# Performance work log

Hardware: AMD Instinct MI355X
Metric: run time of the kernel (lower is better)

The kernel has to match this reference:

```python
import jax, jax.numpy as jnp
import numpy as np

N_NODES = 100000
IN_CH = 256
EMBED = 256
N_EDGES = 300000
EPS = 1e-5


def _glorot(key, shape):
    fan_in, fan_out = shape[0], shape[1]
    lim = (6.0 / (fan_in + fan_out)) ** 0.5
    return jax.random.uniform(key, shape, jnp.float32, -lim, lim)


def setup_inputs() -> dict:
    key = jax.random.key(0)
    ks = jax.random.split(key, 16)
    inp = {}
    inp['node_feat'] = jax.random.normal(ks[0], (N_NODES, IN_CH), jnp.float32)
    inp['src'] = jax.random.randint(ks[1], (N_EDGES,), 0, N_NODES, jnp.int32)
    inp['dst'] = jax.random.randint(ks[2], (N_EDGES,), 0, N_NODES, jnp.int32)
    inp['neg'] = jax.random.randint(ks[3], (N_EDGES,), 0, N_NODES, jnp.int32)
    # GCNConv weights (x @ W + b), 3 layers
    inp['W1'] = _glorot(ks[4], (IN_CH, EMBED)); inp['b1'] = jnp.zeros((EMBED,), jnp.float32)
    inp['W2'] = _glorot(ks[5], (EMBED, EMBED)); inp['b2'] = jnp.zeros((EMBED,), jnp.float32)
    inp['W3'] = _glorot(ks[6], (EMBED, EMBED)); inp['b3'] = jnp.zeros((EMBED,), jnp.float32)
    # BatchNorm affine params (2 BN layers)
    inp['g1'] = jnp.ones((EMBED,), jnp.float32); inp['be1'] = jnp.zeros((EMBED,), jnp.float32)
    inp['g2'] = jnp.ones((EMBED,), jnp.float32); inp['be2'] = jnp.zeros((EMBED,), jnp.float32)
    # LinkPredictor MLP
    inp['fc1_w'] = _glorot(ks[7], (2 * EMBED, EMBED)); inp['fc1_b'] = jnp.zeros((EMBED,), jnp.float32)
    inp['fc2_w'] = _glorot(ks[8], (EMBED, 1)); inp['fc2_b'] = jnp.zeros((1,), jnp.float32)
    return inp


def gcn_conv(x, W, b, src, dst, n):
    # PyG GCNConv: out = D^{-1/2} (A + I) D^{-1/2} (x @ W) + b
    xw = x @ W
    loops = jnp.arange(n, dtype=src.dtype)
    src_l = jnp.concatenate([src, loops])
    dst_l = jnp.concatenate([dst, loops])
    deg = jax.ops.segment_sum(jnp.ones_like(dst_l, jnp.float32), dst_l, num_segments=n)
    dinv = jnp.where(deg > 0, jax.lax.rsqrt(deg), 0.0)
    norm = dinv[src_l] * dinv[dst_l]  # [E+N]
    msg = norm[:, None] * xw[src_l]   # [E+N, d]
    out = jax.ops.segment_sum(msg, dst_l, num_segments=n)
    return out + b


def batch_norm(x, g, b):
    # training-mode BN over node dim, biased variance (torch semantics)
    mu = jnp.mean(x, axis=0)
    var = jnp.mean((x - mu) ** 2, axis=0)
    return (x - mu) * jax.lax.rsqrt(var + EPS) * g + b


def link_pred(z_a, z_b, fc1_w, fc1_b, fc2_w, fc2_b):
    h = jnp.concatenate([z_a, z_b], axis=1) @ fc1_w + fc1_b
    h = jax.nn.relu(h)
    return jax.nn.sigmoid(h @ fc2_w + fc2_b).reshape(-1)


def reference(node_feat, src, dst, neg, W1, b1, W2, b2, W3, b3, g1, be1, g2, be2, fc1_w, fc1_b, fc2_w, fc2_b):
    n = node_feat.shape[0]
    # encoder (dropout p used only in training; inference/deterministic here)
    x = gcn_conv(node_feat, W1, b1, src, dst, n)
    x = jax.nn.relu(batch_norm(x, g1, be1))
    x = gcn_conv(x, W2, b2, src, dst, n)
    x = jax.nn.relu(batch_norm(x, g2, be2))
    z = gcn_conv(x, W3, b3, src, dst, n)
    z_src, z_dst, z_neg = z[src], z[dst], z[neg]
    pos_out = link_pred(z_src, z_dst, fc1_w, fc1_b, fc2_w, fc2_b)
    neg_out = link_pred(z_src, z_neg, fc1_w, fc1_b, fc2_w, fc2_b)
    return (pos_out, neg_out)
```

## Files before the change

kernel.cpp:

```cpp
#include <hip/hip_runtime.h>
#include <hip/hip_bf16.h>

#define N_NODES 100000
#define N_EDGES 300000
#define CH 256
#define EPS 1e-5f
#define AGG_BLOCKS 3125
#define Y_TILES 782
#define Y_TILES_PAD 784
#define CAST_CHUNK 5000

typedef __hip_bfloat16 bf16;
typedef __attribute__((ext_vector_type(8))) short bf16x8_t;
typedef __attribute__((ext_vector_type(4))) float f32x4_t;

__device__ __forceinline__ unsigned short f2bf(float f) {
    bf16 h = __float2bfloat16(f);
    return __builtin_bit_cast(unsigned short, h);
}
__device__ __forceinline__ float bflo(unsigned int w) {
    return __builtin_bit_cast(float, w << 16);
}
__device__ __forceinline__ float bfhi(unsigned int w) {
    return __builtin_bit_cast(float, w & 0xffff0000u);
}
__device__ __forceinline__ unsigned pack2(float a, float b) {
    return (unsigned)f2bf(a) | ((unsigned)f2bf(b) << 16);
}
__device__ __forceinline__ void store_val(bf16* p, float v) { *p = __float2bfloat16(v); }

__device__ __forceinline__ void async_copy16(const void* g, void* l) {
    __builtin_amdgcn_global_load_lds((const __attribute__((address_space(1))) void*)g,
                                     (__attribute__((address_space(3))) void*)l, 16, 0, 0);
}

__device__ __forceinline__ void cast_chunk(const float* __restrict__ x,
                                           unsigned short* __restrict__ y, int i) {
    float4 v = ((const float4*)x)[i];
    ushort4 o;
    o.x = f2bf(v.x); o.y = f2bf(v.y); o.z = f2bf(v.z); o.w = f2bf(v.w);
    ((ushort4*)y)[i] = o;
}

__global__ void k_zero_int(int* __restrict__ p, int n,
                           const float* __restrict__ cx, unsigned short* __restrict__ cy,
                           int castBase, int nbMain) {
    if ((int)blockIdx.x >= nbMain) {
        cast_chunk(cx, cy, (castBase + (int)blockIdx.x - nbMain) * 256 + (int)threadIdx.x);
        return;
    }
    int i = blockIdx.x * 256 + threadIdx.x;
    if (i < n) p[i] = 0;
}
__global__ void k_count_deg(const int* __restrict__ dst, int* __restrict__ deg,
                            const float* __restrict__ cx, unsigned short* __restrict__ cy,
                            int castBase, int nbMain) {
    if ((int)blockIdx.x >= nbMain) {
        cast_chunk(cx, cy, (castBase + (int)blockIdx.x - nbMain) * 256 + (int)threadIdx.x);
        return;
    }
    int e = blockIdx.x * 256 + threadIdx.x;
    if (e < N_EDGES) atomicAdd(&deg[dst[e]], 1);
}
__global__ void k_block_sums(const int* __restrict__ deg, int* __restrict__ bsum,
                             float* __restrict__ dinv,
                             const float* __restrict__ cx, unsigned short* __restrict__ cy,
                             int castBase, int nbMain) {
    if ((int)blockIdx.x >= nbMain) {
        cast_chunk(cx, cy, (castBase + (int)blockIdx.x - nbMain) * 256 + (int)threadIdx.x);
        return;
    }
    __shared__ int s[256];
    int t = threadIdx.x;
    int i = blockIdx.x * 256 + t;
    int v = (i < N_NODES) ? deg[i] : 0;
    s[t] = v;
    if (i < N_NODES) dinv[i] = rsqrtf((float)(v + 1));
    __syncthreads();
    for (int off = 128; off > 0; off >>= 1) {
        if (t < off) s[t] += s[t + off];
        __syncthreads();
    }
    if (t == 0) bsum[blockIdx.x] = s[0];
}
__global__ void k_scan_bsums(int* __restrict__ bsum, int nb) {
    __shared__ int s[512];
    int t = threadIdx.x;
    int v = (t < nb) ? bsum[t] : 0;
    s[t] = v;
    __syncthreads();
    for (int off = 1; off < 512; off <<= 1) {
        int u = (t >= off) ? s[t - off] : 0;
        __syncthreads();
        s[t] += u;
        __syncthreads();
    }
    if (t < nb) bsum[t] = s[t] - v;
}
__global__ void k_row_ptr(const int* __restrict__ deg, const int* __restrict__ bsum,
                          int* __restrict__ row_ptr,
                          const float* __restrict__ cx, unsigned short* __restrict__ cy,
                          int castBase, int nbMain) {
    if ((int)blockIdx.x >= nbMain) {
        cast_chunk(cx, cy, (castBase + (int)blockIdx.x - nbMain) * 256 + (int)threadIdx.x);
        return;
    }
    __shared__ int s[256];
    int t = threadIdx.x;
    int i = blockIdx.x * 256 + t;
    int v = (i < N_NODES) ? deg[i] : 0;
    s[t] = v;
    __syncthreads();
    for (int off = 1; off < 256; off <<= 1) {
        int u = (t >= off) ? s[t - off] : 0;
        __syncthreads();
        s[t] += u;
        __syncthreads();
    }
    if (i < N_NODES) row_ptr[i] = bsum[blockIdx.x] + s[t] - v;
    if (blockIdx.x == 0 && t == 0) row_ptr[N_NODES] = N_EDGES;
}
__global__ void k_scatter(const int* __restrict__ src, const int* __restrict__ dst,
                          const int* __restrict__ row_ptr, int* __restrict__ cursor,
                          const float* __restrict__ dinv,
                          int* __restrict__ col, float* __restrict__ wedge,
                          int* __restrict__ eid, int* __restrict__ rowid,
                          const float* __restrict__ cx, unsigned short* __restrict__ cy,
                          int castBase, int nbMain) {
    if ((int)blockIdx.x >= nbMain) {
        cast_chunk(cx, cy, (castBase + (int)blockIdx.x - nbMain) * 256 + (int)threadIdx.x);
        return;
    }
    int e = blockIdx.x * 256 + threadIdx.x;
    if (e < N_EDGES) {
        int d = dst[e], s = src[e];
        int p = atomicAdd(&cursor[d], 1);
        int idx = row_ptr[d] + p;
        col[idx] = s;
        wedge[idx] = dinv[d] * dinv[s];
        eid[idx] = e;
        rowid[idx] = d;
    }
}

__global__ void k_transpose_all(const float* __restrict__ W1, const float* __restrict__ W2,
                                bf16* __restrict__ wt) {
    int which = blockIdx.x >> 8;
    int idx = ((blockIdx.x & 255) << 8) + threadIdx.x;
    int n = idx >> 8, k = idx & 255;
    const float* W = which ? W2 : W1;
    wt[(size_t)which * 65536 + (size_t)n * 256 + k] =
        __float2bfloat16(W[(size_t)k * 256 + n]);
}

__global__ void k_fuse_w(const float* __restrict__ W3, const float* __restrict__ fc1w,
                         const float* __restrict__ b3, const float* __restrict__ fc1b,
                         bf16* __restrict__ wtf, float* __restrict__ bout) {
    int n = threadIdx.x;
    int nc = n & 255;
    size_t ro = (n < 256) ? 0 : 256;
    if (blockIdx.x == 256) {
        float acc = (n < 256) ? fc1b[n] : 0.f;
#pragma unroll 4
        for (int j = 0; j < 256; ++j)
            acc += b3[j] * fc1w[(ro + j) * 256 + nc];
        bout[n] = acc;
        return;
    }
    __shared__ float w3row[256];
    int k = blockIdx.x;
    if (n < 256) w3row[n] = W3[(size_t)k * 256 + n];
    __syncthreads();
    float acc = 0.f;
#pragma unroll 4
    for (int j = 0; j < 256; ++j)
        acc += w3row[j] * fc1w[(ro + j) * 256 + nc];
    wtf[(size_t)n * 256 + k] = __float2bfloat16(acc);
}

template <int NX, bool BIAS, bool STATS>
__global__ __launch_bounds__(256) void k_gemm_mfma(const bf16* __restrict__ A,
                                                   const bf16* __restrict__ Bt,
                                                   bf16* __restrict__ C, int M, int ldc,
                                                   const float* __restrict__ bias,
                                                   float* __restrict__ part) {
    constexpr int LOG2NX = (NX == 4) ? 2 : 1;
    int id = blockIdx.x;
    int rg = (id & 7) + 8 * (id >> (3 + LOG2NX));
    int ct = (id >> 3) & (NX - 1);
    if (rg >= Y_TILES) return;
    const int row0 = rg * 128;
    const int col0 = ct * 128;

    __shared__ bf16 As[2 * 128 * 64];
    __shared__ bf16 Bs[2 * 128 * 64];
    __shared__ float sS[2][128];
    __shared__ float sQ[2][128];
    const int tid = threadIdx.x;
    const int lane = tid & 63;
    const int w = tid >> 6;
    const int wr = w >> 1, wc = w & 1;
    const int lr = lane & 15, quad = lane >> 4;

    f32x4_t acc[4][4] = {};

    auto issue_ab = [&](int k0, int buf) {
#pragma unroll
        for (int i = 0; i < 4; ++i) {
            int j = i * 256 + tid;
            int r = j >> 3, c = j & 7;
            int gk = ((c ^ (r & 7)) << 3);
            int gr = row0 + r; gr = gr < M ? gr : M - 1;
            async_copy16(A + (size_t)gr * 256 + k0 + gk, (void*)(As + buf * 8192 + j * 8));
            async_copy16(Bt + (size_t)(col0 + r) * 256 + k0 + gk,
                         (void*)(Bs + buf * 8192 + j * 8));
        }
    };
    auto compute = [&](int buf) {
#pragma unroll
        for (int ks = 0; ks < 2; ++ks) {
            bf16x8_t af[4], bfr[4];
#pragma unroll
            for (int mi = 0; mi < 4; ++mi) {
                int m = wr * 64 + mi * 16 + lr;
                int c = (ks * 4 + quad) ^ (m & 7);
                af[mi] = *(const bf16x8_t*)(As + buf * 8192 + m * 64 + c * 8);
            }
#pragma unroll
            for (int ni = 0; ni < 4; ++ni) {
                int n = wc * 64 + ni * 16 + lr;
                int c = (ks * 4 + quad) ^ (n & 7);
                bfr[ni] = *(const bf16x8_t*)(Bs + buf * 8192 + n * 64 + c * 8);
            }
#pragma unroll
            for (int mi = 0; mi < 4; ++mi)
#pragma unroll
                for (int ni = 0; ni < 4; ++ni)
                    acc[mi][ni] = __builtin_amdgcn_mfma_f32_16x16x32_bf16(
                        af[mi], bfr[ni], acc[mi][ni], 0, 0, 0);
        }
    };

    issue_ab(0, 0);

#pragma unroll
    for (int k = 0; k < 4; ++k) {
        const int cur = k & 1;
        if (k < 3) issue_ab((k + 1) * 64, cur ^ 1);
        __builtin_amdgcn_sched_barrier(0);
        if (k < 3) asm volatile("s_waitcnt vmcnt(8)" ::: "memory");
        else asm volatile("s_waitcnt vmcnt(0)" ::: "memory");
        __builtin_amdgcn_sched_barrier(0);
        __builtin_amdgcn_s_barrier();
        compute(cur);
        __builtin_amdgcn_s_barrier();
        __builtin_amdgcn_sched_barrier(0);
    }

#pragma unroll
    for (int ni = 0; ni < 4; ++ni) {
        int colg = col0 + wc * 64 + ni * 16 + lr;
        float bv = BIAS ? bias[colg] : 0.f;
#pragma unroll
        for (int mi = 0; mi < 4; ++mi)
#pragma unroll
            for (int r = 0; r < 4; ++r) acc[mi][ni][r] += bv;
    }
    if (STATS) {
        float cs[4] = {}, cq[4] = {};
#pragma unroll
        for (int mi = 0; mi < 4; ++mi)
#pragma unroll
            for (int r = 0; r < 4; ++r) {
                int row = row0 + wr * 64 + mi * 16 + quad * 4 + r;
                if (row < M) {
#pragma unroll
                    for (int ni = 0; ni < 4; ++ni) {
                        float v = acc[mi][ni][r];
                        cs[ni] += v;
                        cq[ni] += v * v;
                    }
                }
            }
#pragma unroll
        for (int ni = 0; ni < 4; ++ni) {
            cs[ni] += __shfl_xor(cs[ni], 16, 64);
            cs[ni] += __shfl_xor(cs[ni], 32, 64);
            cq[ni] += __shfl_xor(cq[ni], 16, 64);
            cq[ni] += __shfl_xor(cq[ni], 32, 64);
        }
        if (quad == 0) {
#pragma unroll
            for (int ni = 0; ni < 4; ++ni) {
                int cc = wc * 64 + ni * 16 + lr;
                sS[wr][cc] = cs[ni];
                sQ[wr][cc] = cq[ni];
            }
        }
        __syncthreads();
        if (tid < 128) {
            float ss = sS[0][tid] + sS[1][tid];
            float qq = sQ[0][tid] + sQ[1][tid];
            int cg = col0 + tid;
            part[(size_t)rg * 512 + cg] = ss;
            part[(size_t)rg * 512 + 256 + cg] = qq;
        }
    }
#pragma unroll
    for (int mi = 0; mi < 4; ++mi) {
#pragma unroll
        for (int r = 0; r < 4; ++r) {
            int row = row0 + wr * 64 + mi * 16 + quad * 4 + r;
            if (row < M) {
#pragma unroll
                for (int ni = 0; ni < 4; ++ni) {
                    int colg = col0 + wc * 64 + ni * 16 + lr;
                    store_val(C + (size_t)row * ldc + colg, acc[mi][ni][r]);
                }
            }
        }
    }
}

template <bool BN>
__device__ __forceinline__ void expand8(uint4 m, const float* sc, const float* sh, float* r) {
    r[0] = bflo(m.x); r[1] = bfhi(m.x); r[2] = bflo(m.y); r[3] = bfhi(m.y);
    r[4] = bflo(m.z); r[5] = bfhi(m.z); r[6] = bflo(m.w); r[7] = bfhi(m.w);
    if (BN) {
#pragma unroll
        for (int i = 0; i < 8; ++i) r[i] = fmaxf(r[i] * sc[i] + sh[i], 0.f);
    }
}

template <bool BN, bool STATS>
__global__ __launch_bounds__(256) void k_agg_csr(const unsigned short* __restrict__ x,
                                                 const int* __restrict__ row_ptr,
                                                 const int* __restrict__ col,
                                                 const float* __restrict__ wedge,
                                                 const float* __restrict__ dinv,
                                                 const float* __restrict__ scale,
                                                 const float* __restrict__ shift,
                                                 const float* __restrict__ bias,
                                                 bf16* __restrict__ out,
                                                 float* __restrict__ part) {
    __shared__ float sred[8][256];
    __shared__ float qred[8][256];
    int g = threadIdx.x >> 5, lh = threadIdx.x & 31;
    int base = blockIdx.x * 32 + g * 4;
    const uint4* xv = (const uint4*)x;
    float sc[8], sh[8], bs[8];
    if (BN) {
        float4 a = ((const float4*)scale)[lh * 2];
        float4 b = ((const float4*)scale)[lh * 2 + 1];
        float4 c = ((const float4*)shift)[lh * 2];
        float4 d = ((const float4*)shift)[lh * 2 + 1];
        sc[0] = a.x; sc[1] = a.y; sc[2] = a.z; sc[3] = a.w;
        sc[4] = b.x; sc[5] = b.y; sc[6] = b.z; sc[7] = b.w;
        sh[0] = c.x; sh[1] = c.y; sh[2] = c.z; sh[3] = c.w;
        sh[4] = d.x; sh[5] = d.y; sh[6] = d.z; sh[7] = d.w;
    }
    if (STATS) {
        float4 e = ((const float4*)bias)[lh * 2];
        float4 f = ((const float4*)bias)[lh * 2 + 1];
        bs[0] = e.x; bs[1] = e.y; bs[2] = e.z; bs[3] = e.w;
        bs[4] = f.x; bs[5] = f.y; bs[6] = f.z; bs[7] = f.w;
    }
    float s8[8] = {}, q8[8] = {};
#pragma unroll
    for (int n = 0; n < 4; ++n) {
        int node = base + n;
        int beg = row_ptr[node], end = row_ptr[node + 1];
        float dv = dinv[node];
        float s2 = dv * dv;
        uint4 xr = xv[(size_t)node * 32 + lh];
        float rs[8];
        expand8<BN>(xr, sc, sh, rs);
        float a[8];
#pragma unroll
        for (int t = 0; t < 8; ++t) a[t] = s2 * rs[t];
        int i = beg;
        for (; i + 2 <= end; i += 2) {
            int sa = col[i], sb = col[i + 1];
            float wa = wedge[i], wb = wedge[i + 1];
            uint4 ma = xv[(size_t)sa * 32 + lh];
            uint4 mb = xv[(size_t)sb * 32 + lh];
            float ra[8], rb[8];
            expand8<BN>(ma, sc, sh, ra);
            expand8<BN>(mb, sc, sh, rb);
#pragma unroll
            for (int t = 0; t < 8; ++t) a[t] += wa * ra[t] + wb * rb[t];
        }
        if (i < end) {
            int sa = col[i];
            float wa = wedge[i];
            uint4 ma = xv[(size_t)sa * 32 + lh];
            float ra[8];
            expand8<BN>(ma, sc, sh, ra);
#pragma unroll
            for (int t = 0; t < 8; ++t) a[t] += wa * ra[t];
        }
        if (STATS) {
#pragma unroll
            for (int t = 0; t < 8; ++t) {
                a[t] += bs[t];
                s8[t] += a[t];
                q8[t] += a[t] * a[t];
            }
        }
        uint4 o;
        o.x = pack2(a[0], a[1]); o.y = pack2(a[2], a[3]);
        o.z = pack2(a[4], a[5]); o.w = pack2(a[6], a[7]);
        ((uint4*)(out + (size_t)node * CH))[lh] = o;
    }
    if (STATS) {
#pragma unroll
        for (int j = 0; j < 8; ++j) {
            sred[g][lh * 8 + j] = s8[j];
            qred[g][lh * 8 + j] = q8[j];
        }
        __syncthreads();
        int t = threadIdx.x;
        float ss = 0.f, qq = 0.f;
#pragma unroll
        for (int gg = 0; gg < 8; ++gg) {
            ss += sred[gg][t];
            qq += qred[gg][t];
        }
        part[(size_t)blockIdx.x * 512 + t] = ss;
        part[(size_t)blockIdx.x * 512 + 256 + t] = qq;
    }
}

__global__ __launch_bounds__(256) void k_bn_finalize(const float* __restrict__ part,
                                                     const float* __restrict__ g,
                                                     const float* __restrict__ be,
                                                     float* __restrict__ scale,
                                                     float* __restrict__ shift, int npart) {
    int wave = threadIdx.x >> 6, lane = threadIdx.x & 63;
    int c = blockIdx.x * 4 + wave;
    float s = 0.f, q = 0.f;
    for (int j = lane; j < npart; j += 64) {
        s += part[(size_t)j * 512 + c];
        q += part[(size_t)j * 512 + 256 + c];
    }
#pragma unroll
    for (int off = 32; off > 0; off >>= 1) {
        s += __shfl_down(s, off, 64);
        q += __shfl_down(q, off, 64);
    }
    if (lane == 0) {
        float mu = s * (1.0f / N_NODES);
        float var = q * (1.0f / N_NODES) - mu * mu;
        float sc = g[c] * rsqrtf(var + EPS);
        scale[c] = sc;
        shift[c] = be[c] - mu * sc;
    }
}

__global__ __launch_bounds__(256) void k_edge_score(
        const unsigned short* __restrict__ uv,
        const int* __restrict__ col, const int* __restrict__ eid,
        const int* __restrict__ rowid, const int* __restrict__ neg,
        const float* __restrict__ fc2_w, const float* __restrict__ fc2_b,
        float* __restrict__ out) {
    constexpr int NWG = 18750;
    constexpr int Q = NWG / 8, R = NWG % 8;
    int bid = blockIdx.x;
    int xcd = bid & 7, ord = bid >> 3;
    int swz = ((xcd < R) ? xcd * (Q + 1) : R * (Q + 1) + (xcd - R) * Q) + ord;
    int wave = threadIdx.x >> 6, lane = threadIdx.x & 63;
    int qtr = lane >> 4, l = lane & 15;
    int i = swz * 16 + wave * 4 + qtr;
    int s = col[i], d = rowid[i], e = eid[i];
    int g = neg[e];
    const uint4* uvv = (const uint4*)uv;
    uint4 u0 = uvv[(size_t)s * 64 + l * 2];
    uint4 u1 = uvv[(size_t)s * 64 + l * 2 + 1];
    uint4 p0 = uvv[(size_t)d * 64 + 32 + l * 2];
    uint4 p1 = uvv[(size_t)d * 64 + 33 + l * 2];
    uint4 n0 = uvv[(size_t)g * 64 + 32 + l * 2];
    uint4 n1 = uvv[(size_t)g * 64 + 33 + l * 2];
    float4 w0 = ((const float4*)fc2_w)[l * 4];
    float4 w1 = ((const float4*)fc2_w)[l * 4 + 1];
    float4 w2 = ((const float4*)fc2_w)[l * 4 + 2];
    float4 w3 = ((const float4*)fc2_w)[l * 4 + 3];

    float t0 = bflo(u0.x), t1 = bfhi(u0.x), t2 = bflo(u0.y), t3 = bfhi(u0.y);
    float t4 = bflo(u0.z), t5 = bfhi(u0.z), t6 = bflo(u0.w), t7 = bfhi(u0.w);
    float t8 = bflo(u1.x), t9 = bfhi(u1.x), ta = bflo(u1.y), tb = bfhi(u1.y);
    float tc = bflo(u1.z), td = bfhi(u1.z), te = bflo(u1.w), tf = bfhi(u1.w);

    float accp =
        fmaxf(t0 + bflo(p0.x), 0.f) * w0.x + fmaxf(t1 + bfhi(p0.x), 0.f) * w0.y +
        fmaxf(t2 + bflo(p0.y), 0.f) * w0.z + fmaxf(t3 + bfhi(p0.y), 0.f) * w0.w +
        fmaxf(t4 + bflo(p0.z), 0.f) * w1.x + fmaxf(t5 + bfhi(p0.z), 0.f) * w1.y +
        fmaxf(t6 + bflo(p0.w), 0.f) * w1.z + fmaxf(t7 + bfhi(p0.w), 0.f) * w1.w +
        fmaxf(t8 + bflo(p1.x), 0.f) * w2.x + fmaxf(t9 + bfhi(p1.x), 0.f) * w2.y +
        fmaxf(ta + bflo(p1.y), 0.f) * w2.z + fmaxf(tb + bfhi(p1.y), 0.f) * w2.w +
        fmaxf(tc + bflo(p1.z), 0.f) * w3.x + fmaxf(td + bfhi(p1.z), 0.f) * w3.y +
        fmaxf(te + bflo(p1.w), 0.f) * w3.z + fmaxf(tf + bfhi(p1.w), 0.f) * w3.w;
    float accn =
        fmaxf(t0 + bflo(n0.x), 0.f) * w0.x + fmaxf(t1 + bfhi(n0.x), 0.f) * w0.y +
        fmaxf(t2 + bflo(n0.y), 0.f) * w0.z + fmaxf(t3 + bfhi(n0.y), 0.f) * w0.w +
        fmaxf(t4 + bflo(n0.z), 0.f) * w1.x + fmaxf(t5 + bfhi(n0.z), 0.f) * w1.y +
        fmaxf(t6 + bflo(n0.w), 0.f) * w1.z + fmaxf(t7 + bfhi(n0.w), 0.f) * w1.w +
        fmaxf(t8 + bflo(n1.x), 0.f) * w2.x + fmaxf(t9 + bfhi(n1.x), 0.f) * w2.y +
        fmaxf(ta + bflo(n1.y), 0.f) * w2.z + fmaxf(tb + bfhi(n1.y), 0.f) * w2.w +
        fmaxf(tc + bflo(n1.z), 0.f) * w3.x + fmaxf(td + bfhi(n1.z), 0.f) * w3.y +
        fmaxf(te + bflo(n1.w), 0.f) * w3.z + fmaxf(tf + bfhi(n1.w), 0.f) * w3.w;
#pragma unroll
    for (int off = 8; off > 0; off >>= 1) {
        accp += __shfl_down(accp, off, 64);
        accn += __shfl_down(accn, off, 64);
    }
    if (l == 0) {
        float bb = fc2_b[0];
        out[e] = 1.0f / (1.0f + expf(-(accp + bb)));
        out[N_EDGES + e] = 1.0f / (1.0f + expf(-(accn + bb)));
    }
}

extern "C" void kernel_launch(void* const* d_in, const int* in_sizes, int n_in,
                              void* d_out, int out_size, void* d_ws, size_t ws_size,
                              hipStream_t stream) {
    const float* node_feat = (const float*)d_in[0];
    const int* src = (const int*)d_in[1];
    const int* dst = (const int*)d_in[2];
    const int* neg = (const int*)d_in[3];
    const float* W1 = (const float*)d_in[4];  const float* b1 = (const float*)d_in[5];
    const float* W2 = (const float*)d_in[6];  const float* b2 = (const float*)d_in[7];
    const float* W3 = (const float*)d_in[8];  const float* b3 = (const float*)d_in[9];
    const float* g1 = (const float*)d_in[10]; const float* be1 = (const float*)d_in[11];
    const float* g2 = (const float*)d_in[12]; const float* be2 = (const float*)d_in[13];
    const float* fc1_w = (const float*)d_in[14]; const float* fc1_b = (const float*)d_in[15];
    const float* fc2_w = (const float*)d_in[16]; const float* fc2_b = (const float*)d_in[17];
    float* out = (float*)d_out;

    const size_t NF = (size_t)N_NODES * CH;
    bf16* UV = (bf16*)d_ws;
    bf16* Xbf = UV + 2 * NF;
    bf16* XwBf = Xbf + NF;
    bf16* wt = XwBf + NF;
    float* dinv = (float*)(wt + 4 * 65536);
    float* bnpart = dinv + N_NODES;
    float* scale = bnpart + (size_t)AGG_BLOCKS * 512;
    float* shift = scale + CH;
    float* b3fc = shift + CH;
    float* wedge = b3fc + 512;
    int* ideg = (int*)(wedge + N_EDGES);
    int* cursor = ideg + N_NODES;
    int* row_ptr = cursor + N_NODES;
    int* col = row_ptr + N_NODES + 1;
    int* eid = col + N_EDGES;
    int* rowid = eid + N_EDGES;
    int* bsum = rowid + N_EDGES;
    (void)ws_size;

    int gemmBlocks = 2 * Y_TILES_PAD;
    int uvBlocks = 4 * Y_TILES_PAD;
    int nodeBlocks = (N_NODES + 255) / 256;
    int edgeBlocks = (N_EDGES + 255) / 256;
    int zeroBlocks = (2 * N_NODES + 255) / 256;
    int scoreBlocks = N_EDGES / 16;
    unsigned short* Xc = (unsigned short*)Xbf;

    k_zero_int<<<zeroBlocks + CAST_CHUNK, 256, 0, stream>>>(
        ideg, 2 * N_NODES, node_feat, Xc, 0 * CAST_CHUNK, zeroBlocks);
    k_count_deg<<<edgeBlocks + CAST_CHUNK, 256, 0, stream>>>(
        dst, ideg, node_feat, Xc, 1 * CAST_CHUNK, edgeBlocks);
    k_block_sums<<<nodeBlocks + CAST_CHUNK, 256, 0, stream>>>(
        ideg, bsum, dinv, node_feat, Xc, 2 * CAST_CHUNK, nodeBlocks);
    k_scan_bsums<<<1, 512, 0, stream>>>(bsum, nodeBlocks);
    k_row_ptr<<<nodeBlocks + CAST_CHUNK, 256, 0, stream>>>(
        ideg, bsum, row_ptr, node_feat, Xc, 3 * CAST_CHUNK, nodeBlocks);
    k_scatter<<<edgeBlocks + CAST_CHUNK, 256, 0, stream>>>(
        src, dst, row_ptr, cursor, dinv, col, wedge, eid, rowid,
        node_feat, Xc, 4 * CAST_CHUNK, edgeBlocks);

    k_transpose_all<<<512, 256, 0, stream>>>(W1, W2, wt);
    k_fuse_w<<<257, 512, 0, stream>>>(W3, fc1_w, b3, fc1_b, wt + 2 * 65536, b3fc);

    k_gemm_mfma<2, false, false><<<gemmBlocks, 256, 0, stream>>>(
        Xbf, wt, XwBf, N_NODES, 256, nullptr, nullptr);
    k_agg_csr<false, true><<<AGG_BLOCKS, 256, 0, stream>>>(
        (unsigned short*)XwBf, row_ptr, col, wedge, dinv, nullptr, nullptr, b1, Xbf, bnpart);
    k_bn_finalize<<<64, 256, 0, stream>>>(bnpart, g1, be1, scale, shift, AGG_BLOCKS);

    k_agg_csr<true, false><<<AGG_BLOCKS, 256, 0, stream>>>(
        (unsigned short*)Xbf, row_ptr, col, wedge, dinv, scale, shift, nullptr, XwBf, nullptr);
    k_gemm_mfma<2, true, true><<<gemmBlocks, 256, 0, stream>>>(
        XwBf, wt + 65536, Xbf, N_NODES, 256, b2, bnpart);
    k_bn_finalize<<<64, 256, 0, stream>>>(bnpart, g2, be2, scale, shift, Y_TILES);

    k_agg_csr<true, false><<<AGG_BLOCKS, 256, 0, stream>>>(
        (unsigned short*)Xbf, row_ptr, col, wedge, dinv, scale, shift, nullptr, XwBf, nullptr);
    k_gemm_mfma<4, true, false><<<uvBlocks, 256, 0, stream>>>(
        XwBf, wt + 2 * 65536, UV, N_NODES, 512, b3fc, nullptr);

    k_edge_score<<<scoreBlocks, 256, 0, stream>>>((unsigned short*)UV, col, eid, rowid, neg,
                                                  fc2_w, fc2_b, out);
}
```

Before: 575.8 us.

## Restructure MFMA GEMM to 8 waves with single-buffered LDS tiles

The bf16 MFMA GEMM now runs 512 threads per block, so each wave computes a 32x64 sub-tile instead of 64x64. The hand-scheduled double-buffered async-copy pipeline is replaced by a plain single-buffer loop that loads, syncs, computes and syncs again. The aim is to halve LDS use per block and raise occupancy, with launch_bounds(512,6) requesting more resident blocks. In exchange the kernel loses its copy/compute overlap and adds barriers per k-step, and the tight register budget may force spills.

```diff
diff --git a/kernel.cpp b/kernel.cpp
--- a/kernel.cpp
+++ b/kernel.cpp
@@ -179,11 +179,11 @@
 }
 
 template <int NX, bool BIAS, bool STATS>
-__global__ __launch_bounds__(256) void k_gemm_mfma(const bf16* __restrict__ A,
-                                                   const bf16* __restrict__ Bt,
-                                                   bf16* __restrict__ C, int M, int ldc,
-                                                   const float* __restrict__ bias,
-                                                   float* __restrict__ part) {
+__global__ __launch_bounds__(512, 6) void k_gemm_mfma(const bf16* __restrict__ A,
+                                                      const bf16* __restrict__ Bt,
+                                                      bf16* __restrict__ C, int M, int ldc,
+                                                      const float* __restrict__ bias,
+                                                      float* __restrict__ part) {
     constexpr int LOG2NX = (NX == 4) ? 2 : 1;
     int id = blockIdx.x;
     int rg = (id & 7) + 8 * (id >> (3 + LOG2NX));
@@ -192,87 +192,69 @@
     const int row0 = rg * 128;
     const int col0 = ct * 128;
 
-    __shared__ bf16 As[2 * 128 * 64];
-    __shared__ bf16 Bs[2 * 128 * 64];
-    __shared__ float sS[2][128];
-    __shared__ float sQ[2][128];
+    __shared__ bf16 As[128 * 64];
+    __shared__ bf16 Bs[128 * 64];
+    __shared__ float sS[4][128];
+    __shared__ float sQ[4][128];
     const int tid = threadIdx.x;
     const int lane = tid & 63;
     const int w = tid >> 6;
     const int wr = w >> 1, wc = w & 1;
     const int lr = lane & 15, quad = lane >> 4;
 
-    f32x4_t acc[4][4] = {};
-
-    auto issue_ab = [&](int k0, int buf) {
-#pragma unroll
-        for (int i = 0; i < 4; ++i) {
-            int j = i * 256 + tid;
+    f32x4_t acc[2][4] = {};
+
+    for (int k0 = 0; k0 < 256; k0 += 64) {
+#pragma unroll
+        for (int i = 0; i < 2; ++i) {
+            int j = i * 512 + tid;
             int r = j >> 3, c = j & 7;
             int gk = ((c ^ (r & 7)) << 3);
             int gr = row0 + r; gr = gr < M ? gr : M - 1;
-            async_copy16(A + (size_t)gr * 256 + k0 + gk, (void*)(As + buf * 8192 + j * 8));
-            async_copy16(Bt + (size_t)(col0 + r) * 256 + k0 + gk,
-                         (void*)(Bs + buf * 8192 + j * 8));
-        }
-    };
-    auto compute = [&](int buf) {
+            async_copy16(A + (size_t)gr * 256 + k0 + gk, (void*)(As + j * 8));
+            async_copy16(Bt + (size_t)(col0 + r) * 256 + k0 + gk, (void*)(Bs + j * 8));
+        }
+        __syncthreads();
 #pragma unroll
         for (int ks = 0; ks < 2; ++ks) {
-            bf16x8_t af[4], bfr[4];
-#pragma unroll
-            for (int mi = 0; mi < 4; ++mi) {
-                int m = wr * 64 + mi * 16 + lr;
+            bf16x8_t af[2], bfr[4];
+#pragma unroll
+            for (int mi = 0; mi < 2; ++mi) {
+                int m = wr * 32 + mi * 16 + lr;
                 int c = (ks * 4 + quad) ^ (m & 7);
-                af[mi] = *(const bf16x8_t*)(As + buf * 8192 + m * 64 + c * 8);
+                af[mi] = *(const bf16x8_t*)(As + m * 64 + c * 8);
             }
 #pragma unroll
             for (int ni = 0; ni < 4; ++ni) {
                 int n = wc * 64 + ni * 16 + lr;
                 int c = (ks * 4 + quad) ^ (n & 7);
-                bfr[ni] = *(const bf16x8_t*)(Bs + buf * 8192 + n * 64 + c * 8);
+                bfr[ni] = *(const bf16x8_t*)(Bs + n * 64 + c * 8);
             }
 #pragma unroll
-            for (int mi = 0; mi < 4; ++mi)
+            for (int mi = 0; mi < 2; ++mi)
 #pragma unroll
                 for (int ni = 0; ni < 4; ++ni)
                     acc[mi][ni] = __builtin_amdgcn_mfma_f32_16x16x32_bf16(
                         af[mi], bfr[ni], acc[mi][ni], 0, 0, 0);
         }
-    };
-
-    issue_ab(0, 0);
-
-#pragma unroll
-    for (int k = 0; k < 4; ++k) {
-        const int cur = k & 1;
-        if (k < 3) issue_ab((k + 1) * 64, cur ^ 1);
-        __builtin_amdgcn_sched_barrier(0);
-        if (k < 3) asm volatile("s_waitcnt vmcnt(8)" ::: "memory");
-        else asm volatile("s_waitcnt vmcnt(0)" ::: "memory");
-        __builtin_amdgcn_sched_barrier(0);
-        __builtin_amdgcn_s_barrier();
-        compute(cur);
-        __builtin_amdgcn_s_barrier();
-        __builtin_amdgcn_sched_barrier(0);
-    }
-
+        __syncthreads();
+    }
 #pragma unroll
     for (int ni = 0; ni < 4; ++ni) {
         int colg = col0 + wc * 64 + ni * 16 + lr;
         float bv = BIAS ? bias[colg] : 0.f;
 #pragma unroll
-        for (int mi = 0; mi < 4; ++mi)
+        for (int mi = 0; mi < 2; ++mi)
 #pragma unroll
             for (int r = 0; r < 4; ++r) acc[mi][ni][r] += bv;
     }
     if (STATS) {
         float cs[4] = {}, cq[4] = {};
 #pragma unroll
-        for (int mi = 0; mi < 4; ++mi)
+        for (int mi = 0; mi < 2; ++mi)
 #pragma unroll
             for (int r = 0; r < 4; ++r) {
-                int row = row0 + wr * 64 + mi * 16 + quad * 4 + r;
+                int row = row0 + wr * 32 + mi * 16 + quad * 4 + r;
                 if (row < M) {
 #pragma unroll
                     for (int ni = 0; ni < 4; ++ni) {
@@ -299,18 +281,18 @@
         }
         __syncthreads();
         if (tid < 128) {
-            float ss = sS[0][tid] + sS[1][tid];
-            float qq = sQ[0][tid] + sQ[1][tid];
+            float ss = sS[0][tid] + sS[1][tid] + sS[2][tid] + sS[3][tid];
+            float qq = sQ[0][tid] + sQ[1][tid] + sQ[2][tid] + sQ[3][tid];
             int cg = col0 + tid;
             part[(size_t)rg * 512 + cg] = ss;
             part[(size_t)rg * 512 + 256 + cg] = qq;
         }
     }
 #pragma unroll
-    for (int mi = 0; mi < 4; ++mi) {
+    for (int mi = 0; mi < 2; ++mi) {
 #pragma unroll
         for (int r = 0; r < 4; ++r) {
-            int row = row0 + wr * 64 + mi * 16 + quad * 4 + r;
+            int row = row0 + wr * 32 + mi * 16 + quad * 4 + r;
             if (row < M) {
 #pragma unroll
                 for (int ni = 0; ni < 4; ++ni) {
@@ -580,7 +562,7 @@
     k_transpose_all<<<512, 256, 0, stream>>>(W1, W2, wt);
     k_fuse_w<<<257, 512, 0, stream>>>(W3, fc1_w, b3, fc1_b, wt + 2 * 65536, b3fc);
 
-    k_gemm_mfma<2, false, false><<<gemmBlocks, 256, 0, stream>>>(
+    k_gemm_mfma<2, false, false><<<gemmBlocks, 512, 0, stream>>>(
         Xbf, wt, XwBf, N_NODES, 256, nullptr, nullptr);
     k_agg_csr<false, true><<<AGG_BLOCKS, 256, 0, stream>>>(
         (unsigned short*)XwBf, row_ptr, col, wedge, dinv, nullptr, nullptr, b1, Xbf, bnpart);
@@ -588,13 +570,13 @@
 
     k_agg_csr<true, false><<<AGG_BLOCKS, 256, 0, stream>>>(
         (unsigned short*)Xbf, row_ptr, col, wedge, dinv, scale, shift, nullptr, XwBf, nullptr);
-    k_gemm_mfma<2, true, true><<<gemmBlocks, 256, 0, stream>>>(
+    k_gemm_mfma<2, true, true><<<gemmBlocks, 512, 0, stream>>>(
         XwBf, wt + 65536, Xbf, N_NODES, 256, b2, bnpart);
     k_bn_finalize<<<64, 256, 0, stream>>>(bnpart, g2, be2, scale, shift, Y_TILES);
 
     k_agg_csr<true, false><<<AGG_BLOCKS, 256, 0, stream>>>(
         (unsigned short*)Xbf, row_ptr, col, wedge, dinv, scale, shift, nullptr, XwBf, nullptr);
-    k_gemm_mfma<4, true, false><<<uvBlocks, 256, 0, stream>>>(
+    k_gemm_mfma<4, true, false><<<uvBlocks, 512, 0, stream>>>(
         XwBf, wt + 2 * 65536, UV, N_NODES, 512, b3fc, nullptr);
 
     k_edge_score<<<scoreBlocks, 256, 0, stream>>>((unsigned short*)UV, col, eid, rowid, neg,
```

Result: faster. 551.3 us (median of 3 runs) (-4.3%).
